# Kernel optimization log

Hardware: AMD Instinct MI355X
Metric: run time of the kernel (lower is better)

The kernel has to match this reference:

```python
import jax, jax.numpy as jnp
from jax import lax
import numpy as np

COMMITMENT_COST = 0.25
DATA_VARIANCE = 1.0
DN = ('NCHW', 'OIHW', 'NCHW')


def _conv(x, w, b, stride, pad):
    y = lax.conv_general_dilated(x, w, (stride, stride), ((pad, pad), (pad, pad)), dimension_numbers=DN)
    return y + b[None, :, None, None]


def _conv_t(x, w, b, stride, pad, out_pad):
    # PyTorch ConvTranspose2d(w: [Cin, Cout, kH, kW]) == dilated conv with flipped, transposed kernel
    wf = jnp.flip(w, (2, 3)).transpose(1, 0, 2, 3)  # -> [Cout, Cin, kH, kW]
    k = w.shape[2]
    lo, hi = k - 1 - pad, k - 1 - pad + out_pad
    y = lax.conv_general_dilated(x, wf, (1, 1), ((lo, hi), (lo, hi)), lhs_dilation=(stride, stride), dimension_numbers=DN)
    return y + b[None, :, None, None]


def setup_inputs() -> dict:
    key = jax.random.key(0)
    ks = jax.random.split(key, 14)
    n = lambda k, shp, s: (jax.random.normal(k, shp, dtype=jnp.float32) * s)
    return {
        'x': n(ks[0], (64, 3, 256, 256), 1.0),
        'enc_w1': n(ks[1], (32, 3, 3, 3), 0.2), 'enc_b1': n(ks[2], (32,), 0.02),
        'enc_w2': n(ks[3], (64, 32, 3, 3), 0.06), 'enc_b2': n(ks[4], (64,), 0.02),
        'enc_w3': n(ks[5], (16, 64, 1, 1), 0.12), 'enc_b3': n(ks[6], (16,), 0.02),
        'codebook': n(ks[7], (512, 16), 1.0),
        'dec_w1': n(ks[8], (16, 64, 3, 3), 0.08), 'dec_b1': n(ks[9], (64,), 0.02),
        'dec_w2': n(ks[10], (64, 32, 3, 3), 0.04), 'dec_b2': n(ks[11], (32,), 0.02),
        'dec_w3': n(ks[12], (32, 3, 3, 3), 0.06), 'dec_b3': n(ks[13], (3,), 0.02),
    }


def reference(x, enc_w1, enc_b1, enc_w2, enc_b2, enc_w3, enc_b3, codebook,
              dec_w1, dec_b1, dec_w2, dec_b2, dec_w3, dec_b3):
    # Encoder: 3 -> 32 (s2) -> 64 (s2) -> D (1x1)
    z = jax.nn.relu(_conv(x, enc_w1, enc_b1, 2, 1))
    z = jax.nn.relu(_conv(z, enc_w2, enc_b2, 2, 1))
    z = _conv(z, enc_w3, enc_b3, 1, 0)  # [B, D, H/4, W/4]

    # Vector quantization (training path)
    zp = z.transpose(0, 2, 3, 1)                      # [B, h, w, D]
    D = zp.shape[-1]
    flat = zp.reshape(-1, D)                          # [N, D]
    dist = (jnp.sum(flat * flat, axis=1, keepdims=True)
            + jnp.sum(codebook * codebook, axis=1)
            - 2.0 * flat @ codebook.T)                # [N, K]
    idx = jnp.argmin(dist, axis=1)                    # [N]
    quantized = codebook[idx].reshape(zp.shape)       # [B, h, w, D]

    q_latent_loss = jnp.mean((quantized - lax.stop_gradient(zp)) ** 2)
    e_latent_loss = jnp.mean((zp - lax.stop_gradient(quantized)) ** 2)
    e_q_loss = q_latent_loss + COMMITMENT_COST * e_latent_loss

    ste = zp + lax.stop_gradient(quantized - zp)      # straight-through
    e = ste.transpose(0, 3, 1, 2)                     # [B, D, h, w]

    # Decoder: D -> 64 (x2) -> 32 (x2) -> 3
    y = jax.nn.relu(_conv_t(e, dec_w1, dec_b1, 2, 1, 1))
    y = jax.nn.relu(_conv_t(y, dec_w2, dec_b2, 2, 1, 1))
    x_recon = _conv_t(y, dec_w3, dec_b3, 1, 1, 0)

    recon_mse = jnp.mean((x_recon - x) ** 2)
    recon_loss = recon_mse / DATA_VARIANCE
    return jnp.stack([e_q_loss, recon_loss, recon_mse])
```

## Files before the change

### kernel.cpp

```cpp
#include <hip/hip_runtime.h>
#include <hip/hip_bf16.h>


typedef __attribute__((ext_vector_type(8))) short bf16x8;
typedef __attribute__((ext_vector_type(4))) float f32x4;
typedef unsigned short ushort_t;

__device__ __forceinline__ ushort_t f2bf(float v) {
    __hip_bfloat16 h = __float2bfloat16(v);
    return *(ushort_t*)&h;
}
__device__ __forceinline__ float bf2f(ushort_t u) {
    __hip_bfloat16 h = *(__hip_bfloat16*)&u;
    return __bfloat162float(h);
}
__device__ __forceinline__ unsigned pack2r(float a, float b) {
    return (unsigned)f2bf(fmaxf(a, 0.f)) | ((unsigned)f2bf(fmaxf(b, 0.f)) << 16);
}
__device__ __forceinline__ int xcd_chunk(int flat, int nwg) {
    return (flat & 7) * (nwg >> 3) + (flat >> 3);
}


__global__ void zero_k(float* __restrict__ acc) {
    acc[blockIdx.x * 256 + threadIdx.x] = 0.f;
}

__global__ __launch_bounds__(256) void prep_k(
        const float* __restrict__ ew1, const float* __restrict__ ew2,
        const float* __restrict__ dw1, const float* __restrict__ dw2,
        const float* __restrict__ dw3, const float* __restrict__ cb,
        ushort_t* __restrict__ wt, float* __restrict__ cn) {
    int idx = blockIdx.x * 256 + threadIdx.x;
    if (idx < 1024) {
        int co = idx >> 5, k = idx & 31;
        wt[idx] = (k < 27) ? f2bf(ew1[co * 27 + k]) : (ushort_t)0;
    } else if (idx < 19456) {
        int i = idx - 1024;
        int t = i >> 11, co = (i >> 5) & 63, ci = i & 31;
        int lci = ((ci & 1) << 4) | (ci >> 1);
        wt[idx] = f2bf(ew2[co * 288 + lci * 9 + t]);
    } else if (idx < 37888) {
        int i = idx - 19456;
        int t = i >> 11, co = (i >> 5) & 63, k = i & 31;
        wt[idx] = (k < 16) ? f2bf(dw1[k * 576 + co * 9 + t]) : (ushort_t)0;
    } else if (idx < 56320) {
        int i = idx - 37888;
        int t = i >> 11, kc = (i >> 10) & 1, co = (i >> 5) & 31, ci = i & 31;
        int m = kc * 32 + ci;
        int lci = ((m & 3) << 4) | (m >> 2);
        wt[idx] = f2bf(dw2[lci * 288 + co * 9 + t]);
    } else if (idx < 60928) {
        int i = idx - 56320;
        int t = i >> 9, co = (i >> 5) & 15, ci = i & 31;
        int lci = ((ci & 1) << 4) | (ci >> 1);
        wt[idx] = (co < 3) ? f2bf(dw3[lci * 27 + co * 9 + (8 - t)]) : (ushort_t)0;
    } else if (idx < 61440) {
        int k = idx - 60928;
        float s = 0.f;
        #pragma unroll
        for (int d = 0; d < 16; ++d) { float v = cb[k * 16 + d]; s += v * v; }
        cn[k] = s;
    }
}

__global__ __launch_bounds__(256) void pad_k(ushort_t* __restrict__ d1p) {
    const int img = blockIdx.x, tid = threadIdx.x;
    const uint4 z = (uint4){0, 0, 0, 0};
    uint4* b1 = (uint4*)(d1p + (size_t)img * 1065024);
    for (int i = tid; i < 1032; i += 256) b1[132096 + i] = z;
    for (int i = tid; i < 1024; i += 256) {
        int r = i >> 3, u = i & 7;
        b1[(r * 129 + 128) * 8 + u] = z;
    }
}

__global__ __launch_bounds__(256, 4) void conv1_k(const float* __restrict__ x,
        const ushort_t* __restrict__ wt, const float* __restrict__ bias,
        ushort_t* __restrict__ a1) {
    const int L = xcd_chunk(blockIdx.y, gridDim.y);
    const int b = L >> 7, oh = L & 127;
    const int tid = threadIdx.x;
    __shared__ __align__(16) ushort_t sX[9 * 264];
    __shared__ int sOff[32];
    for (int i = tid; i < 9 * 264 / 2; i += 256) ((unsigned*)sX)[i] = 0u;
    if (tid < 32) {
        int k = tid, off = 0;
        if (k < 27) { int ci = k / 9, r9 = k % 9, kh = r9 / 3, kw = r9 % 3;
                      off = (ci * 3 + kh) * 264 + kw; }
        sOff[tid] = off;
    }
    __syncthreads();
    #pragma unroll
    for (int it = 0; it < 9; ++it) {
        int slot = it * 256 + tid;
        int ci = slot / 768, r = slot % 768, kh = r >> 8, iw = r & 255;
        int ih = 2 * oh + kh - 1;
        float v = ((unsigned)ih < 256u) ? x[(long)(b * 3 + ci) * 65536 + ih * 256 + iw] : 0.f;
        sX[(ci * 3 + kh) * 264 + iw + 1] = f2bf(v);
    }
    __syncthreads();
    const int lane = tid & 63, wave = tid >> 6, q = lane >> 4, n16 = lane & 15;
    bf16x8 Bw[2];
    #pragma unroll
    for (int u = 0; u < 2; ++u)
        Bw[u] = *(const bf16x8*)(wt + (u * 16 + n16) * 32 + q * 8);
    f32x4 acc[2][2];
    #pragma unroll
    for (int u = 0; u < 2; ++u) {
        float bz = bias[u * 16 + n16];
        acc[0][u] = (f32x4){bz, bz, bz, bz};
        acc[1][u] = (f32x4){bz, bz, bz, bz};
    }
    #pragma unroll
    for (int mf = 0; mf < 2; ++mf) {
        const int m2 = 2 * (wave * 32 + mf * 16 + n16);
        ushort_t av[8];
        #pragma unroll
        for (int j = 0; j < 8; ++j) {
            int k = q * 8 + j;
            av[j] = (k < 27) ? sX[sOff[k] + m2] : (ushort_t)0;
        }
        bf16x8 A = *(bf16x8*)av;
        #pragma unroll
        for (int u = 0; u < 2; ++u)
            acc[mf][u] = __builtin_amdgcn_mfma_f32_16x16x32_bf16(A, Bw[u], acc[mf][u], 0, 0, 0);
    }
    #pragma unroll
    for (int mf = 0; mf < 2; ++mf)
        #pragma unroll
        for (int r = 0; r < 4; ++r) {
            int ow = wave * 32 + mf * 16 + q * 4 + r;
            *(unsigned*)(a1 + ((long)(b * 128 + oh) * 128 + ow) * 32 + n16 * 2) =
                pack2r(acc[mf][0][r], acc[mf][1][r]);
        }
}

__global__ __launch_bounds__(256, 4) void conv2_k(const ushort_t* __restrict__ a1,
        const ushort_t* __restrict__ wt, const float* __restrict__ bias,
        ushort_t* __restrict__ a2) {
    const int L = xcd_chunk(blockIdx.y, gridDim.y);
    const int b = L >> 6, oh = L & 63;
    const int tid = threadIdx.x;
    __shared__ __align__(16) ushort_t sA[3 * 2 * 66 * 40];
    uint4* z4 = (uint4*)sA;
    #pragma unroll
    for (int it = 0; it < 8; ++it) {
        int slot = it * 256 + tid;
        if (slot < 1980) z4[slot] = (uint4){0, 0, 0, 0};
    }
    __syncthreads();
    #pragma unroll
    for (int it = 0; it < 6; ++it) {
        int slot = it * 256 + tid;
        if (slot < 1536) {
            int kh = slot >> 9, rem = slot & 511, iw = rem >> 2, ci8 = (rem & 3) << 3;
            int ih = 2 * oh + kh - 1;
            if ((unsigned)ih < 128u) {
                uint4 v = *(const uint4*)(a1 + ((long)(b * 128 + ih) * 128 + iw) * 32 + ci8);
                int idx = iw + 2, p = idx & 1, c = idx >> 1;
                *(uint4*)&sA[((kh * 2 + p) * 66 + c) * 40 + ci8] = v;
            }
        }
    }
    __syncthreads();
    const int lane = tid & 63, wave = tid >> 6, q = lane >> 4, n16 = lane & 15;
    f32x4 acc[4];
    #pragma unroll
    for (int u = 0; u < 4; ++u) {
        float bz = bias[u * 16 + n16];
        acc[u] = (f32x4){bz, bz, bz, bz};
    }
    const int ow = wave * 16 + n16;
    #pragma unroll
    for (int t = 0; t < 9; ++t) {
        const int kh = t / 3, kw = t % 3;
        const int p = (kw == 1) ? 0 : 1;
        const int c = (kw == 0) ? ow : ow + 1;
        bf16x8 A = *(bf16x8*)&sA[((kh * 2 + p) * 66 + c) * 40 + q * 8];
        #pragma unroll
        for (int u = 0; u < 4; ++u) {
            bf16x8 B = *(const bf16x8*)(wt + 1024 + t * 2048 + (u * 16 + n16) * 32 + q * 8);
            acc[u] = __builtin_amdgcn_mfma_f32_16x16x32_bf16(A, B, acc[u], 0, 0, 0);
        }
    }
    #pragma unroll
    for (int r = 0; r < 4; ++r) {
        int owo = wave * 16 + q * 4 + r;
        uint2 pk;
        pk.x = pack2r(acc[0][r], acc[1][r]);
        pk.y = pack2r(acc[2][r], acc[3][r]);
        *(uint2*)(a2 + ((long)(b * 64 + oh) * 64 + owo) * 64 + n16 * 4) = pk;
    }
}

__global__ __launch_bounds__(256) void conv3_vq_k(const ushort_t* __restrict__ a2,
        const float* __restrict__ w3, const float* __restrict__ b3,
        const float* __restrict__ cb, const float* __restrict__ cn,
        ushort_t* __restrict__ e, float* __restrict__ acc) {
    const int base = blockIdx.x * 512 + threadIdx.x;
    __shared__ float sred[4];
    float z[2][16];
    #pragma unroll
    for (int p = 0; p < 2; ++p)
        #pragma unroll
        for (int d = 0; d < 16; ++d) z[p][d] = b3[d];
    #pragma unroll
    for (int p = 0; p < 2; ++p) {
        const ushort_t* arow = a2 + (long)(base + p * 256) * 64;
        #pragma unroll
        for (int c8 = 0; c8 < 8; ++c8) {
            uint4 raw = *(const uint4*)(arow + c8 * 8);
            ushort_t us[8];
            *(uint4*)us = raw;
            #pragma unroll
            for (int j = 0; j < 8; ++j) {
                int m = c8 * 8 + j;
                int lci = ((m & 3) << 4) | (m >> 2);
                float a = bf2f(us[j]);
                #pragma unroll
                for (int d = 0; d < 16; ++d)
                    z[p][d] = fmaf(a, w3[d * 64 + lci], z[p][d]);
            }
        }
    }
    const float4* cb4 = (const float4*)cb;
    float best0 = 1e30f, best1 = 1e30f; int bi0 = 0, bi1 = 0;
    for (int k = 0; k < 512; ++k) {
        float4 c0 = cb4[k * 4 + 0], c1 = cb4[k * 4 + 1];
        float4 c2 = cb4[k * 4 + 2], c3 = cb4[k * 4 + 3];
        float nk = cn[k];
        float d0 = z[0][0]*c0.x + z[0][1]*c0.y + z[0][2]*c0.z + z[0][3]*c0.w
                 + z[0][4]*c1.x + z[0][5]*c1.y + z[0][6]*c1.z + z[0][7]*c1.w
                 + z[0][8]*c2.x + z[0][9]*c2.y + z[0][10]*c2.z + z[0][11]*c2.w
                 + z[0][12]*c3.x + z[0][13]*c3.y + z[0][14]*c3.z + z[0][15]*c3.w;
        float d1 = z[1][0]*c0.x + z[1][1]*c0.y + z[1][2]*c0.z + z[1][3]*c0.w
                 + z[1][4]*c1.x + z[1][5]*c1.y + z[1][6]*c1.z + z[1][7]*c1.w
                 + z[1][8]*c2.x + z[1][9]*c2.y + z[1][10]*c2.z + z[1][11]*c2.w
                 + z[1][12]*c3.x + z[1][13]*c3.y + z[1][14]*c3.z + z[1][15]*c3.w;
        float dist0 = nk - 2.f * d0, dist1 = nk - 2.f * d1;
        if (dist0 < best0) { best0 = dist0; bi0 = k; }
        if (dist1 < best1) { best1 = dist1; bi1 = k; }
    }
    float lsum = 0.f;
    #pragma unroll
    for (int d = 0; d < 16; ++d) {
        float q0 = cb[bi0 * 16 + d], q1 = cb[bi1 * 16 + d];
        float f0 = q0 - z[0][d], f1 = q1 - z[1][d];
        lsum += f0 * f0 + f1 * f1;
        e[(long)base * 16 + d] = f2bf(q0);
        e[(long)(base + 256) * 16 + d] = f2bf(q1);
    }
    #pragma unroll
    for (int off = 32; off > 0; off >>= 1) lsum += __shfl_down(lsum, off, 64);
    if ((threadIdx.x & 63) == 0) sred[threadIdx.x >> 6] = lsum;
    __syncthreads();
    if (threadIdx.x == 0)
        atomicAdd(&acc[(blockIdx.x & 63) << 5],
                  sred[0] + sred[1] + sred[2] + sred[3]);
}

__global__ __launch_bounds__(256, 4) void dec1_k(const ushort_t* __restrict__ e,
        const ushort_t* __restrict__ wt, const float* __restrict__ bias,
        ushort_t* __restrict__ d1p) {
    const int L = xcd_chunk(blockIdx.y, gridDim.y);
    const int b = L >> 6, i = L & 63;
    const int tid = threadIdx.x;
    __shared__ __align__(16) ushort_t sE[2 * 66 * 24];
    uint4* z4 = (uint4*)sE;
    #pragma unroll
    for (int it = 0; it < 2; ++it) {
        int slot = it * 256 + tid;
        if (slot < 396) z4[slot] = (uint4){0, 0, 0, 0};
    }
    __syncthreads();
    {
        int dh = tid >> 7, rem = tid & 127, j = rem >> 1, ci8 = (rem & 1) * 8;
        if (i + dh < 64) {
            uint4 v = *(const uint4*)(e + ((long)((b * 64 + i + dh) * 64 + j)) * 16 + ci8);
            *(uint4*)&sE[(dh * 66 + j) * 24 + ci8] = v;
        }
    }
    __syncthreads();
    const int lane = tid & 63, wave = tid >> 6, q = lane >> 4, n16 = lane & 15;
    f32x4 acc[4][4];
    #pragma unroll
    for (int u = 0; u < 4; ++u) {
        float bz = bias[u * 16 + n16];
        #pragma unroll
        for (int c = 0; c < 4; ++c) acc[c][u] = (f32x4){bz, bz, bz, bz};
    }
    const int jl = wave * 16 + n16;
    #pragma unroll
    for (int t = 0; t < 9; ++t) {
        const int kh = t / 3, kw = t % 3;
        const int dh = (kh == 0) ? 1 : 0, dw = (kw == 0) ? 1 : 0;
        const int cls = ((kh != 1) ? 2 : 0) | ((kw != 1) ? 1 : 0);
        bf16x8 A = *(bf16x8*)&sE[(dh * 66 + jl + dw) * 24 + (q & 1) * 8];
        #pragma unroll
        for (int u = 0; u < 4; ++u) {
            bf16x8 B = *(const bf16x8*)(wt + 19456 + t * 2048 + (u * 16 + n16) * 32 + q * 8);
            acc[cls][u] = __builtin_amdgcn_mfma_f32_16x16x32_bf16(A, B, acc[cls][u], 0, 0, 0);
        }
    }
    #pragma unroll
    for (int ph = 0; ph < 2; ++ph)
        #pragma unroll
        for (int pw = 0; pw < 2; ++pw)
            #pragma unroll
            for (int r = 0; r < 4; ++r) {
                int oh = 2 * i + ph;
                int ow = 2 * (wave * 16 + q * 4 + r) + pw;
                uint2 pk;
                pk.x = pack2r(acc[ph * 2 + pw][0][r], acc[ph * 2 + pw][1][r]);
                pk.y = pack2r(acc[ph * 2 + pw][2][r], acc[ph * 2 + pw][3][r]);
                *(uint2*)(d1p + (size_t)b * 1065024 + ((long)oh * 129 + ow) * 64 + n16 * 4) = pk;
            }
}

__global__ __launch_bounds__(256, 3) void dec23_k(const ushort_t* __restrict__ d1p,
        const ushort_t* __restrict__ wt, const float* __restrict__ db2,
        const float* __restrict__ db3, const float* __restrict__ x,
        float* __restrict__ acc) {
    const int flat = blockIdx.y * 2 + blockIdx.x;
    const int L = xcd_chunk(flat, gridDim.y * 2);
    const int bx = L & 1, byl = L >> 1;
    const int b = byl >> 6, i4 = byl & 63;
    const int j0 = bx << 7;
    const int tid = threadIdx.x;
    const int lane = tid & 63, wave = tid >> 6, q = lane >> 4, n16 = lane & 15;

    __shared__ __align__(16) ushort_t sT[6 * 132 * 32];
    __shared__ float sred[4];
    uint4* z4 = (uint4*)sT;
    #pragma unroll
    for (int it = 0; it < 13; ++it) {
        int s = it * 256 + tid;
        if (s < 3168) z4[s] = (uint4){0, 0, 0, 0};
    }
    __syncthreads();

    const int bb0 = (j0 >> 1) - 1;
    const ushort_t* dbase = d1p + (size_t)b * 1065024;
    const int aidx = wave;
    const int a = 2 * i4 + aidx - 1;
    const bool doP0 = (aidx != 0);
    const bool doP1 = (aidx != 3);
    int r0 = a, r1 = a + 1;
    r0 = ((unsigned)r0 <= 128u) ? r0 : 128;
    r1 = ((unsigned)r1 <= 128u) ? r1 : 128;
    const ushort_t* rowp0 = dbase + (long)r0 * 8256;
    const ushort_t* rowp1 = dbase + (long)r1 * 8256;
    int colo[5][2];
    #pragma unroll
    for (int cell = 0; cell < 5; ++cell)
        #pragma unroll
        for (int dw = 0; dw < 2; ++dw) {
            int col = bb0 + cell * 16 + n16 + dw;
            colo[cell][dw] = (((unsigned)col <= 128u) ? col : 128) * 64;
        }
    const float bz0 = db2[n16], bz1 = db2[16 + n16];
    f32x4 a5[2][5];

#define INIT5()                                                                     \
    _Pragma("unroll")                                                               \
    for (int cell = 0; cell < 5; ++cell) {                                          \
        a5[0][cell] = (f32x4){bz0, bz0, bz0, bz0};                                  \
        a5[1][cell] = (f32x4){bz1, bz1, bz1, bz1};                                  \
    }
#define TAP5(T, DH, DW)                                                             \
    {                                                                               \
        const ushort_t* wb = wt + 37888 + (T) * 2048;                               \
        const ushort_t* rp = (DH) ? rowp1 : rowp0;                                  \
        _Pragma("unroll")                                                           \
        for (int kc = 0; kc < 2; ++kc) {                                            \
            bf16x8 B0 = *(const bf16x8*)(wb + kc * 1024 + n16 * 32 + q * 8);        \
            bf16x8 B1 = *(const bf16x8*)(wb + kc * 1024 + (16 + n16) * 32 + q * 8); \
            _Pragma("unroll")                                                       \
            for (int cell = 0; cell < 5; ++cell) {                                  \
                bf16x8 Av = *(const bf16x8*)(rp + colo[cell][DW] + kc * 32 + q * 8);\
                a5[0][cell] = __builtin_amdgcn_mfma_f32_16x16x32_bf16(              \
                    Av, B0, a5[0][cell], 0, 0, 0);                                  \
                a5[1][cell] = __builtin_amdgcn_mfma_f32_16x16x32_bf16(              \
                    Av, B1, a5[1][cell], 0, 0, 0);                                  \
            }                                                                       \
        }                                                                           \
    }
#define EPI5(PH, PW)                                                                \
    {                                                                               \
        int R = 2 * a + (PH);                                                       \
        if ((unsigned)R < 256u) {                                                   \
            int Rp = R - 4 * i4 + 1;                                                \
            _Pragma("unroll")                                                       \
            for (int cell = 0; cell < 5; ++cell)                                    \
                _Pragma("unroll")                                                   \
                for (int r = 0; r < 4; ++r) {                                       \
                    int lq = cell * 16 + q * 4 + r;                                 \
                    int cp = 2 * lq + (PW) - 1;                                     \
                    int cg = 2 * (bb0 + lq) + (PW);                                 \
                    if ((unsigned)cg < 256u && (unsigned)cp < 130u)                 \
                        *(unsigned*)&sT[Rp * 4224 + cp * 32 + n16 * 2] =            \
                            pack2r(a5[0][cell][r], a5[1][cell][r]);                 \
                }                                                                   \
        }                                                                           \
    }
    if (doP0) {
        INIT5(); TAP5(4, 0, 0); EPI5(0, 0);
        INIT5(); TAP5(3, 0, 1); TAP5(5, 0, 0); EPI5(0, 1);
    }
    if (doP1) {
        INIT5(); TAP5(1, 1, 0); TAP5(7, 0, 0); EPI5(1, 0);
        INIT5(); TAP5(0, 1, 1); TAP5(2, 1, 0); TAP5(6, 0, 1); TAP5(8, 0, 0);
        EPI5(1, 1);
    }
#undef INIT5
#undef TAP5
#undef EPI5
    __syncthreads();

    bf16x8 Bw[9];
    #pragma unroll
    for (int t = 0; t < 9; ++t)
        Bw[t] = *(const bf16x8*)(wt + 56320 + t * 512 + n16 * 32 + q * 8);
    float bz3 = (n16 < 3) ? db3[n16] : 0.f;
    f32x4 a4[8];
    #pragma unroll
    for (int mf = 0; mf < 8; ++mf) a4[mf] = (f32x4){bz3, bz3, bz3, bz3};
    const int oh = 4 * i4 + wave;
    #pragma unroll
    for (int kh = 0; kh < 3; ++kh) {
        const ushort_t* srow = &sT[(wave + kh) * 4224];
        #pragma unroll
        for (int mf = 0; mf < 8; ++mf) {
            #pragma unroll
            for (int kw = 0; kw < 3; ++kw) {
                bf16x8 A = *(const bf16x8*)(srow + (mf * 16 + n16 + kw) * 32 + q * 8);
                a4[mf] = __builtin_amdgcn_mfma_f32_16x16x32_bf16(A, Bw[kh * 3 + kw], a4[mf], 0, 0, 0);
            }
        }
    }
    float lsum = 0.f;
    if (n16 < 3) {
        const float* xrow = x + ((long)(b * 3 + n16) * 256 + oh) * 256 + j0;
        #pragma unroll
        for (int mf = 0; mf < 8; ++mf)
            #pragma unroll
            for (int r = 0; r < 4; ++r) {
                int ow = mf * 16 + q * 4 + r;
                float df = a4[mf][r] - xrow[ow];
                lsum += df * df;
            }
    }
    #pragma unroll
    for (int off = 32; off > 0; off >>= 1) lsum += __shfl_down(lsum, off, 64);
    if (lane == 0) sred[wave] = lsum;
    __syncthreads();
    if (tid == 0)
        atomicAdd(&acc[2048 + ((byl & 63) << 5)],
                  sred[0] + sred[1] + sred[2] + sred[3]);
}

__global__ void finalize_k(const float* __restrict__ acc, float* __restrict__ out) {
    int t = threadIdx.x;
    float v = acc[t << 5];
    float m = acc[2048 + (t << 5)];
    #pragma unroll
    for (int off = 32; off > 0; off >>= 1) {
        v += __shfl_down(v, off, 64);
        m += __shfl_down(m, off, 64);
    }
    if (t == 0) {
        float eq  = 1.25f * v / 4194304.f;
        float mse = m / 12582912.f;
        out[0] = eq;
        out[1] = mse;
        out[2] = mse;
    }
}

extern "C" void kernel_launch(void* const* d_in, const int* in_sizes, int n_in,
                              void* d_out, int out_size, void* d_ws, size_t ws_size,
                              hipStream_t stream) {
    (void)in_sizes; (void)n_in; (void)out_size;
    const float* x   = (const float*)d_in[0];
    const float* ew1 = (const float*)d_in[1];
    const float* eb1 = (const float*)d_in[2];
    const float* ew2 = (const float*)d_in[3];
    const float* eb2 = (const float*)d_in[4];
    const float* ew3 = (const float*)d_in[5];
    const float* eb3 = (const float*)d_in[6];
    const float* cb  = (const float*)d_in[7];
    const float* dw1 = (const float*)d_in[8];
    const float* db1 = (const float*)d_in[9];
    const float* dw2 = (const float*)d_in[10];
    const float* db2 = (const float*)d_in[11];
    const float* dw3 = (const float*)d_in[12];
    const float* db3 = (const float*)d_in[13];
    float* out = (float*)d_out;

    int C = 64;
    while (C > 1 && (size_t)147456 + (size_t)C * 2261120UL > ws_size) C >>= 1;

    char* base = (char*)d_ws;
    float*    acc = (float*)base;
    ushort_t* wt  = (ushort_t*)(base + 16384);
    float*    cn  = (float*)(base + 16384 + 121856);
    ushort_t* e   = (ushort_t*)(base + 147456);
    char*     rgn = base + 147456 + (size_t)C * 131072UL;
    ushort_t* a1  = (ushort_t*)rgn;
    ushort_t* a2  = (ushort_t*)(rgn + (size_t)C * 1048576UL);
    ushort_t* d1p = (ushort_t*)rgn;

    zero_k<<<16, 256, 0, stream>>>(acc);
    prep_k<<<240, 256, 0, stream>>>(ew1, ew2, dw1, dw2, dw3, cb, wt, cn);

    for (int b0 = 0; b0 < 64; b0 += C) {
        const float* xc = x + (size_t)b0 * 196608UL;
        conv1_k   <<<dim3(1, C * 128), 256, 0, stream>>>(xc,  wt, eb1, a1);
        conv2_k   <<<dim3(1, C * 64),  256, 0, stream>>>(a1,  wt, eb2, a2);
        conv3_vq_k<<<dim3(C * 8),      256, 0, stream>>>(a2,  ew3, eb3, cb, cn, e, acc);
        pad_k     <<<dim3(C),          256, 0, stream>>>(d1p);
        dec1_k    <<<dim3(1, C * 64),  256, 0, stream>>>(e,   wt, db1, d1p);
        dec23_k   <<<dim3(2, C * 64),  256, 0, stream>>>(d1p, wt, db2, db3, xc, acc);
    }
    finalize_k<<<1, 64, 0, stream>>>(acc, out);
}
```

Before: 656.4 us.

## Reuse LDS A-fragments across kw taps via DPP row rotation in dec23

The final 3x3 convolution in dec23_k now loads each A fragment from LDS once per kh (the centre tap) and builds the kw=0 and kw=2 shifted fragments with DPP row rotations, patching only the boundary lanes from two edge loads. This cuts LDS reads for that loop by roughly a factor of three. Weight fragments are now loaded per kh instead of all nine up front, which lowers register pressure. The LDS zeroing is also narrowed to the halo columns and to the top and bottom rows at image edges only, on the assumption that the interior is fully overwritten later. The DPP lane logic adds VALU work and correctness risk if the rotation semantics or the halo assumptions are off.

```diff
diff --git a/kernel.cpp b/kernel.cpp
--- a/kernel.cpp
+++ b/kernel.cpp
@@ -4,6 +4,7 @@
 
 typedef __attribute__((ext_vector_type(8))) short bf16x8;
 typedef __attribute__((ext_vector_type(4))) float f32x4;
+typedef __attribute__((ext_vector_type(4))) int i32x4;
 typedef unsigned short ushort_t;
 
 __device__ __forceinline__ ushort_t f2bf(float v) {
@@ -20,6 +21,15 @@
 __device__ __forceinline__ int xcd_chunk(int flat, int nwg) {
     return (flat & 7) * (nwg >> 3) + (flat >> 3);
 }
+#define ROR_FRAG(dst, src, CTRL)                                        \
+    {                                                                   \
+        i32x4 _a = __builtin_bit_cast(i32x4, src), _r;                  \
+        _r[0] = __builtin_amdgcn_mov_dpp(_a[0], CTRL, 0xF, 0xF, false); \
+        _r[1] = __builtin_amdgcn_mov_dpp(_a[1], CTRL, 0xF, 0xF, false); \
+        _r[2] = __builtin_amdgcn_mov_dpp(_a[2], CTRL, 0xF, 0xF, false); \
+        _r[3] = __builtin_amdgcn_mov_dpp(_a[3], CTRL, 0xF, 0xF, false); \
+        dst = __builtin_bit_cast(bf16x8, _r);                           \
+    }
 
 
 __global__ void zero_k(float* __restrict__ acc) {
@@ -332,11 +342,18 @@
 
     __shared__ __align__(16) ushort_t sT[6 * 132 * 32];
     __shared__ float sred[4];
-    uint4* z4 = (uint4*)sT;
-    #pragma unroll
-    for (int it = 0; it < 13; ++it) {
-        int s = it * 256 + tid;
-        if (s < 3168) z4[s] = (uint4){0, 0, 0, 0};
+
+    {
+        unsigned* sw = (unsigned*)sT;
+        if (tid < 96) {
+            int r6 = tid >> 4, w16 = tid & 15;
+            int c = (bx == 0) ? 0 : 129;
+            sw[r6 * 2112 + c * 16 + w16] = 0u;
+        }
+        if (i4 == 0)
+            for (int i = tid; i < 2080; i += 256) sw[i] = 0u;
+        if (i4 == 63)
+            for (int i = tid; i < 2080; i += 256) sw[5 * 2112 + i] = 0u;
     }
     __syncthreads();
 
@@ -418,25 +435,42 @@
 #undef EPI5
     __syncthreads();
 
-    bf16x8 Bw[9];
-    #pragma unroll
-    for (int t = 0; t < 9; ++t)
-        Bw[t] = *(const bf16x8*)(wt + 56320 + t * 512 + n16 * 32 + q * 8);
     float bz3 = (n16 < 3) ? db3[n16] : 0.f;
     f32x4 a4[8];
     #pragma unroll
     for (int mf = 0; mf < 8; ++mf) a4[mf] = (f32x4){bz3, bz3, bz3, bz3};
     const int oh = 4 * i4 + wave;
+    const bool is_l0 = (n16 == 0), is_l15 = (n16 == 15);
     #pragma unroll
     for (int kh = 0; kh < 3; ++kh) {
         const ushort_t* srow = &sT[(wave + kh) * 4224];
+        bf16x8 Bk0 = *(const bf16x8*)(wt + 56320 + (kh * 3 + 0) * 512 + n16 * 32 + q * 8);
+        bf16x8 Bk1 = *(const bf16x8*)(wt + 56320 + (kh * 3 + 1) * 512 + n16 * 32 + q * 8);
+        bf16x8 Bk2 = *(const bf16x8*)(wt + 56320 + (kh * 3 + 2) * 512 + n16 * 32 + q * 8);
+        bf16x8 G[8];
+        #pragma unroll
+        for (int mf = 0; mf < 8; ++mf)
+            G[mf] = *(const bf16x8*)(srow + (mf * 16 + n16 + 1) * 32 + q * 8);
+        bf16x8 E  = *(const bf16x8*)(srow + n16 * 32 + q * 8);
+        bf16x8 E2 = *(const bf16x8*)(srow + (114 + n16) * 32 + q * 8);
+        #pragma unroll
+        for (int mf = 0; mf < 8; ++mf)
+            a4[mf] = __builtin_amdgcn_mfma_f32_16x16x32_bf16(G[mf], Bk1, a4[mf], 0, 0, 0);
+        bf16x8 P = E;
         #pragma unroll
         for (int mf = 0; mf < 8; ++mf) {
-            #pragma unroll
-            for (int kw = 0; kw < 3; ++kw) {
-                bf16x8 A = *(const bf16x8*)(srow + (mf * 16 + n16 + kw) * 32 + q * 8);
-                a4[mf] = __builtin_amdgcn_mfma_f32_16x16x32_bf16(A, Bw[kh * 3 + kw], a4[mf], 0, 0, 0);
-            }
+            bf16x8 Qm; ROR_FRAG(Qm, G[mf], 0x121);
+            bf16x8 kw0 = is_l0 ? P : Qm;
+            a4[mf] = __builtin_amdgcn_mfma_f32_16x16x32_bf16(kw0, Bk0, a4[mf], 0, 0, 0);
+            P = Qm;
+        }
+        P = E2;
+        #pragma unroll
+        for (int mf = 7; mf >= 0; --mf) {
+            bf16x8 Rm; ROR_FRAG(Rm, G[mf], 0x12F);
+            bf16x8 kw2 = is_l15 ? P : Rm;
+            a4[mf] = __builtin_amdgcn_mfma_f32_16x16x32_bf16(kw2, Bk2, a4[mf], 0, 0, 0);
+            P = Rm;
         }
     }
     float lsum = 0.f;
```

New measurement: 652.7 us. Within noise of the previous version (-0.6%).
